# Kernel tuning notes

Measured on AMD Instinct MI355X. Metric: run time of the kernel, lower is better.

Reference implementation:

```python
import jax, jax.numpy as jnp
import numpy as np

D_MODEL = 1024
N_HEADS = 16
D_K = D_MODEL // N_HEADS
T_MIN = 0.01
T_MAX = 2.0
B = 4
S = 1024


def setup_inputs() -> dict:
    key = jax.random.key(0)
    ks = jax.random.split(key, 16)
    sc = 1.0 / np.sqrt(D_MODEL).astype(np.float32)
    inp = {
        'query': jax.random.normal(ks[0], (B, S, D_MODEL), jnp.float32),
        'key': jax.random.normal(ks[1], (B, S, D_MODEL), jnp.float32),
        'value': jax.random.normal(ks[2], (B, S, D_MODEL), jnp.float32),
        # Linear weights stored as (in, out); torch does x @ W.T + b with W (out,in)
        'Wq': jax.random.normal(ks[3], (D_MODEL, D_MODEL), jnp.float32) * sc,
        'bq': jax.random.normal(ks[4], (D_MODEL,), jnp.float32) * 0.01,
        'Wk': jax.random.normal(ks[5], (D_MODEL, D_MODEL), jnp.float32) * sc,
        'bk': jax.random.normal(ks[6], (D_MODEL,), jnp.float32) * 0.01,
        'Wv': jax.random.normal(ks[7], (D_MODEL, D_MODEL), jnp.float32) * sc,
        'bv': jax.random.normal(ks[8], (D_MODEL,), jnp.float32) * 0.01,
        'Wo': jax.random.normal(ks[9], (D_MODEL, D_MODEL), jnp.float32) * sc,
        'bo': jax.random.normal(ks[10], (D_MODEL,), jnp.float32) * 0.01,
        # time-predictor MLP: Linear(3,16) -> tanh -> Linear(16,1)
        'Wt1': jax.random.normal(ks[11], (3, 16), jnp.float32) * 0.5,
        'bt1': jax.random.normal(ks[12], (16,), jnp.float32) * 0.1,
        'Wt2': jax.random.normal(ks[13], (16, 1), jnp.float32) * 0.25,
        'bt2': jax.random.normal(ks[14], (1,), jnp.float32) * 0.1,
    }
    return inp


def _forward(query, key, value, Wq, bq, Wk, bk, Wv, bv, Wo, bo, Wt1, bt1, Wt2, bt2):
    Bq, Sq, D = query.shape
    Sk = key.shape[1]

    def proj(x, W, b, Slen):
        return (x @ W + b).reshape(Bq, Slen, N_HEADS, D_K).transpose(0, 2, 1, 3)

    Q = proj(query, Wq, bq, Sq)   # (B,H,Sq,dk)
    K = proj(key, Wk, bk, Sk)     # (B,H,Sk,dk)
    V = proj(value, Wv, bv, Sk)   # (B,H,Sk,dk)

    # --- DiffusionTimePredictor (fp32) ---
    Qf = Q.astype(jnp.float32)
    Kf = K.astype(jnp.float32)
    inv_sqrt_dk = np.float32(1.0 / np.sqrt(D_K))
    s = jnp.einsum('bhqd,bhkd->bhqk', Qf, Kf) * inv_sqrt_dk
    s = jnp.clip(s, -50.0, 50.0)
    mean_sim = s.mean(axis=(-2, -1))                       # (B,H)
    max_sim = s.max(axis=-1).mean(axis=-1)                 # (B,H)
    probs = jax.nn.softmax(s / 2.0, axis=-1)
    entropy_proxy = probs.var(axis=-1, ddof=1).mean(axis=-1)  # torch var unbiased=True
    mean_sim = jnp.clip(jnp.nan_to_num(mean_sim), -10.0, 10.0)
    max_sim = jnp.clip(jnp.nan_to_num(max_sim), -10.0, 10.0)
    entropy_proxy = jnp.clip(jnp.nan_to_num(entropy_proxy, nan=0.1), 0.0, 1.0)
    feats = jnp.stack([mean_sim, max_sim, entropy_proxy], axis=-1)  # (B,H,3)
    raw_t = jnp.tanh(feats @ Wt1 + bt1) @ Wt2 + bt2                  # (B,H,1)
    t = T_MIN + jax.nn.sigmoid(raw_t) * (T_MAX - T_MIN)
    t = jnp.clip(t, T_MIN, T_MAX)[..., None].astype(query.dtype)     # (B,H,1,1)
    t = jnp.minimum(t, 0.85)                                          # clamp(max=0.85)

    # --- heat kernel attention ---
    scores = jnp.einsum('bhqd,bhkd->bhqk', Q, K) / (2.0 * t)
    attn = jnp.nan_to_num(jax.nn.softmax(scores, axis=-1))
    out = jnp.einsum('bhqk,bhkd->bhqd', attn, V)
    out = out.transpose(0, 2, 1, 3).reshape(Bq, Sq, D)
    return out @ Wo + bo


def reference(query, key, value, Wq, bq, Wk, bk, Wv, bv, Wo, bo, Wt1, bt1, Wt2, bt2):
    return _forward(query, key, value, Wq, bq, Wk, bk, Wv, bv, Wo, bo, Wt1, bt1, Wt2, bt2)
```

## Files before the change

### kernel.cpp

```cpp
#include <hip/hip_runtime.h>
#include <hip/hip_bf16.h>
#include <math.h>

#define SS   1024
#define DM   1024
#define NH   16
#define DKH  64
#define NB   4
#define NBH  64

typedef unsigned short ush;
typedef unsigned int uint32;
typedef __attribute__((ext_vector_type(8))) short bf8_t;
typedef __attribute__((ext_vector_type(4))) float f32x4;
#define MFMA16(a,b,c) __builtin_amdgcn_mfma_f32_16x16x32_bf16((a),(b),(c),0,0,0)

__device__ __forceinline__ ush f2bf(float x){ return __bfloat16_as_ushort(__float2bfloat16(x)); }
__device__ __forceinline__ float bf2f(ush h){ return __bfloat162float(__ushort_as_bfloat16(h)); }
__device__ __forceinline__ uint32 pk2(float a, float b){
  return (uint32)f2bf(a) | ((uint32)f2bf(b) << 16);
}
__device__ __forceinline__ uint32 pkhl(float v){
  ush h = f2bf(v);
  return (uint32)h | ((uint32)f2bf(v - bf2f(h)) << 16);
}
__device__ __forceinline__ uint32 prmh(uint32 uhi, uint32 ulo){
  return __builtin_amdgcn_perm(uhi, ulo, 0x05040100u);
}
__device__ __forceinline__ uint32 prml(uint32 uhi, uint32 ulo){
  return __builtin_amdgcn_perm(uhi, ulo, 0x07060302u);
}
__device__ __forceinline__ int swz8(int row, int chunk){
  return row*64 + (((chunk) ^ (row & 7)) << 3);
}
union U4B8 { uint4 u; bf8_t b; };

__global__ __launch_bounds__(256) void xconv(
    const float* __restrict__ q, const float* __restrict__ k, const float* __restrict__ v,
    ush* __restrict__ xq, ush* __restrict__ xk, ush* __restrict__ xv)
{
  const float* src = (blockIdx.y==0)?q:(blockIdx.y==1)?k:v;
  ush* dst = (blockIdx.y==0)?xq:(blockIdx.y==1)?xk:xv;
  const size_t i = ((size_t)blockIdx.x*256 + threadIdx.x)*8;
  float4 a = *(const float4*)&src[i];
  float4 b = *(const float4*)&src[i+4];
  uint4 o;
  o.x = pk2(a.x, a.y); o.y = pk2(a.z, a.w);
  o.z = pk2(b.x, b.y); o.w = pk2(b.z, b.w);
  *(uint4*)&dst[i] = o;
}

__global__ void wconv4(const float* __restrict__ W0, const float* __restrict__ W1,
                       const float* __restrict__ W2, const float* __restrict__ W3,
                       ush* __restrict__ H0, ush* __restrict__ H1,
                       ush* __restrict__ H2, ush* __restrict__ H3)
{
  __shared__ float T[32][33];
  const int tx = threadIdx.x, ty = threadIdx.y;
  const int z = blockIdx.z;
  const float* W = (z==0)?W0:(z==1)?W1:(z==2)?W2:W3;
  ush* H = (z==0)?H0:(z==1)?H1:(z==2)?H2:H3;
  const int k0 = blockIdx.y*32, n0 = blockIdx.x*32;
  #pragma unroll
  for (int i = 0; i < 4; ++i){
    int r = ty + 8*i;
    T[r][tx] = W[(size_t)(k0 + r)*DM + n0 + tx];
  }
  __syncthreads();
  #pragma unroll
  for (int i = 0; i < 4; ++i){
    int r = ty + 8*i;
    H[(size_t)(n0 + r)*DM + k0 + tx] = f2bf(T[tx][r]);
  }
}

__global__ __launch_bounds__(256) void proj_qkv(
    const ush* __restrict__ xq, const ush* __restrict__ xk, const ush* __restrict__ xv,
    const ush* __restrict__ Wqh, const ush* __restrict__ Wkh, const ush* __restrict__ Wvh,
    const float* __restrict__ bq, const float* __restrict__ bk,
    const float* __restrict__ bv,
    uint32* __restrict__ Qi, ush* __restrict__ Kb, ush* __restrict__ Vt)
{
  __shared__ ush SMEM[16896];

  const int fid = blockIdx.x;
  const int glob = (fid & 7)*96 + (fid >> 3);
  const int z = glob >> 8, rem = glob & 255;
  const int m0 = (rem >> 3) * 128, n0 = (rem & 7) * 128;

  const ush* A  = (z==0) ? xq  : (z==1) ? xk  : xv;
  const ush* Bh = (z==0) ? Wqh : (z==1) ? Wkh : Wvh;

  const int tid = threadIdx.x;
  const int lane = tid & 63, w = tid >> 6;
  const int c = lane & 15, g = lane >> 4;
  const int wr = w >> 1, wc = w & 1;

  f32x4 acc[4][4];
  #pragma unroll
  for (int i = 0; i < 4; ++i)
    #pragma unroll
    for (int j = 0; j < 4; ++j) acc[i][j] = (f32x4){0.f,0.f,0.f,0.f};

  const int prow0 = w*16 + (lane >> 3), prow1 = prow0 + 8;
  const int jj = lane & 7;
  const int sg0 = jj ^ (prow0 & 7), sg1 = jj ^ (prow1 & 7);
  const size_t aoff0 = (size_t)(2*prow0 + (sg0 >> 2))*DM + (sg0 & 3)*8;
  const size_t aoff1 = (size_t)(2*prow1 + (sg1 >> 2))*DM + (sg1 & 3)*8;
  const ush* Aab = A  + (size_t)m0*DM;
  const ush* Bhb = Bh + (size_t)n0*DM;
  const int lb0 = w*1024, lb1 = w*1024 + 512;

#define GLL(GP, LIDX) __builtin_amdgcn_global_load_lds( \
    (const __attribute__((address_space(1))) unsigned int*)(GP), \
    (__attribute__((address_space(3))) unsigned int*)(&SMEM[LIDX]), 16, 0, 0)

#define ISSUE_PROJ(BUFO, KT) do{ \
    GLL(Aab + aoff0 + (KT), (BUFO) + lb0); \
    GLL(Aab + aoff1 + (KT), (BUFO) + lb1); \
    GLL(Bhb + aoff0 + (KT), (BUFO) + 4096 + lb0); \
    GLL(Bhb + aoff1 + (KT), (BUFO) + 4096 + lb1); \
  }while(0)

  const int csw = (((4*(c & 1) + g) ^ ((c >> 1) & 7)) << 3);

  ISSUE_PROJ(0, 0);
  int cur = 0;
  for (int kt = 0; kt < DM; kt += 32){
    __syncthreads();
    if (kt + 32 < DM) ISSUE_PROJ((cur ^ 1)*8192, kt + 32);

    const ush* As  = SMEM + cur*8192;
    const ush* Bhs = As + 4096;

    bf8_t a_h[4];
    #pragma unroll
    for (int fm = 0; fm < 4; ++fm)
      a_h[fm] = *(const bf8_t*)&As[(32*wr + 8*fm + (c>>1))*64 + csw];
    __builtin_amdgcn_s_setprio(1);
    #pragma unroll
    for (int fn = 0; fn < 4; ++fn){
      bf8_t b_h = *(const bf8_t*)&Bhs[(32*wc + 8*fn + (c>>1))*64 + csw];
      #pragma unroll
      for (int fm = 0; fm < 4; ++fm)
        acc[fm][fn] = MFMA16(a_h[fm], b_h, acc[fm][fn]);
    }
    __builtin_amdgcn_s_setprio(0);
    cur ^= 1;
  }
#undef ISSUE_PROJ
#undef GLL

  if (z == 0){
    #pragma unroll
    for (int fm = 0; fm < 4; ++fm){
      #pragma unroll
      for (int fn = 0; fn < 4; ++fn){
        const int col = n0 + 64*wc + 16*fn + c;
        const float bb = bq[col];
        const int row0 = m0 + 64*wr + 16*fm + 4*g;
        const int hd = col >> 6, d = col & 63;
        #pragma unroll
        for (int r = 0; r < 4; ++r){
          const int row = row0 + r;
          const int b = row >> 10, s = row & 1023;
          Qi[((size_t)(b*NH + hd)*SS + s)*DKH + d] = pkhl(acc[fm][fn][r] + bb);
        }
      }
    }
  } else if (z == 1){
    #pragma unroll
    for (int fm = 0; fm < 4; ++fm){
      #pragma unroll
      for (int fn = 0; fn < 4; ++fn){
        const int col = n0 + 64*wc + 16*fn + c;
        const float bb = bk[col];
        const int row0 = m0 + 64*wr + 16*fm + 4*g;
        const int hd = col >> 6, d = col & 63;
        #pragma unroll
        for (int r = 0; r < 4; ++r){
          const int row = row0 + r;
          const int b = row >> 10, s = row & 1023;
          Kb[((size_t)(b*NH + hd)*SS + s)*DKH + d] = f2bf(acc[fm][fn][r] + bb);
        }
      }
    }
  } else {
    __syncthreads();
    ush* Vep = SMEM + w*4224;
    #pragma unroll
    for (int fm = 0; fm < 4; ++fm){
      #pragma unroll
      for (int fn = 0; fn < 4; ++fn){
        const float bb = bv[n0 + 64*wc + 16*fn + c];
        #pragma unroll
        for (int r = 0; r < 4; ++r)
          Vep[(16*fn + c)*66 + 16*fm + 4*g + r] = f2bf(acc[fm][fn][r] + bb);
      }
    }
    const int b = m0 >> 10;
    const int s0 = (m0 & 1023) + 64*wr;
    const int hd = (n0 >> 6) + wc;
    const size_t vbase = ((size_t)(b*NH + hd))*DKH*SS;
    #pragma unroll
    for (int it = 0; it < 8; ++it){
      const int dr = 8*it + (lane >> 3);
      const int sc = (lane & 7)*8;
      uint4 vv = *(const uint4*)&Vep[dr*66 + sc];
      *(uint4*)&Vt[vbase + (size_t)dr*SS + s0 + sc] = vv;
    }
  }
}

__global__ __launch_bounds__(256) void gemm_out(
    const ush* __restrict__ Abf, const ush* __restrict__ Bth,
    const float* __restrict__ bias, float* __restrict__ outf)
{
  __shared__ ush As[4096], Bs[2048];

  const int fid = blockIdx.x;
  const int glob = (fid & 7)*64 + (fid >> 3);
  const int m0 = (glob >> 4)*128, n0 = (glob & 15)*64;

  const int tid = threadIdx.x;
  const int lane = tid & 63, w = tid >> 6;
  const int c = lane & 15, g = lane >> 4;
  const int wr = w >> 1, wc = w & 1;

  f32x4 acc[4][2];
  #pragma unroll
  for (int i = 0; i < 4; ++i){ acc[i][0] = (f32x4){0,0,0,0}; acc[i][1] = (f32x4){0,0,0,0}; }

  const int prow = tid >> 3, ci = tid & 7;
  const int lr   = 2*prow + (ci >> 2);
  const int koff = (ci & 3) << 3;
  const int ws0  = prow*64 + ((ci ^ (prow & 7)) << 3);
  const int ws1  = ws0 + 32*64;
  const int csw  = (((4*(c & 1) + g) ^ ((c >> 1) & 7)) << 3);

  uint4 ar0, ar1, brr;
  #define ISSUE_OUT(KT) do{ \
    ar0 = *(const uint4*)(Abf + (size_t)(m0 + lr)*DM + (KT) + koff); \
    ar1 = *(const uint4*)(Abf + (size_t)(m0 + lr + 64)*DM + (KT) + koff); \
    brr = *(const uint4*)(Bth + (size_t)(n0 + lr)*DM + (KT) + koff); \
  }while(0)

  ISSUE_OUT(0);
  for (int kt = 0; kt < DM; kt += 32){
    *(uint4*)&As[ws0] = ar0;
    *(uint4*)&As[ws1] = ar1;
    if (lr < 64) *(uint4*)&Bs[ws0] = brr;
    __syncthreads();
    if (kt + 32 < DM) ISSUE_OUT(kt + 32);

    bf8_t a_h[4];
    #pragma unroll
    for (int fm = 0; fm < 4; ++fm)
      a_h[fm] = *(const bf8_t*)&As[(32*wr + 8*fm + (c>>1))*64 + csw];
    #pragma unroll
    for (int fn = 0; fn < 2; ++fn){
      bf8_t b_h = *(const bf8_t*)&Bs[(16*wc + 8*fn + (c>>1))*64 + csw];
      #pragma unroll
      for (int fm = 0; fm < 4; ++fm)
        acc[fm][fn] = MFMA16(a_h[fm], b_h, acc[fm][fn]);
    }
    __syncthreads();
  }
  #undef ISSUE_OUT

  #pragma unroll
  for (int fm = 0; fm < 4; ++fm){
    #pragma unroll
    for (int fn = 0; fn < 2; ++fn){
      const int col = n0 + 32*wc + 16*fn + c;
      const float bb = bias[col];
      const int row0 = m0 + 64*wr + 16*fm + 4*g;
      #pragma unroll
      for (int r = 0; r < 4; ++r)
        outf[(size_t)(row0 + r)*DM + col] = acc[fm][fn][r] + bb;
    }
  }
}

__global__ __launch_bounds__(512) void attn_stats_mfma(
    const uint32* __restrict__ Qi, const ush* __restrict__ Kb,
    float* __restrict__ stats, unsigned int* __restrict__ cnt,
    const float* __restrict__ Wt1, const float* __restrict__ bt1,
    const float* __restrict__ Wt2, const float* __restrict__ bt2,
    float* __restrict__ tws)
{
  __shared__ ush Khs[128*64];
  __shared__ float red[8][3];
  const int tid = threadIdx.x, lane = tid & 63, w = tid >> 6;
  const int c = lane & 15, g = lane >> 4;
  const int fid = blockIdx.x;
  const int glob = (fid & 7)*64 + (fid >> 3);
  const int bh = glob >> 3, q0 = (glob & 7)*128;

  bf8_t qh[2];
  {
    const size_t qoff = ((size_t)bh*SS + q0 + 16*w + c)*DKH + 8*g;
    uint4 u0 = *(const uint4*)(Qi + qoff);
    uint4 u1 = *(const uint4*)(Qi + qoff + 4);
    uint4 u2 = *(const uint4*)(Qi + qoff + 32);
    uint4 u3 = *(const uint4*)(Qi + qoff + 36);
    U4B8 t;
    t.u = (uint4){prmh(u0.y,u0.x), prmh(u0.w,u0.z), prmh(u1.y,u1.x), prmh(u1.w,u1.z)}; qh[0] = t.b;
    t.u = (uint4){prmh(u2.y,u2.x), prmh(u2.w,u2.z), prmh(u3.y,u3.x), prmh(u3.w,u3.z)}; qh[1] = t.b;
  }

  float ssum = 0.f, rmax = -1e30f, lsum = 0.f, l2sum = 0.f;
  const int rrK = tid >> 2, chK = (tid & 3)*2;

  uint4 k0, k1;
  #define ISSUE_ST(KC) do{ \
    const ush* kp = Kb + ((size_t)bh*SS + (KC)*128 + rrK)*DKH + chK*8; \
    k0 = *(const uint4*)(kp); \
    k1 = *(const uint4*)(kp + 8); \
  }while(0)

  ISSUE_ST(0);
  for (int kc = 0; kc < 8; ++kc){
    *(uint4*)&Khs[rrK*64 + (((chK + 0) ^ (rrK & 7)) << 3)] = k0;
    *(uint4*)&Khs[rrK*64 + (((chK + 1) ^ (rrK & 7)) << 3)] = k1;
    __syncthreads();
    if (kc < 7) ISSUE_ST(kc + 1);

    f32x4 sa[8];
    #pragma unroll
    for (int fn = 0; fn < 8; ++fn) sa[fn] = (f32x4){0.f,0.f,0.f,0.f};
    __builtin_amdgcn_s_setprio(1);
    #pragma unroll
    for (int fn = 0; fn < 8; ++fn){
      #pragma unroll
      for (int ds = 0; ds < 2; ++ds){
        bf8_t ah = *(const bf8_t*)&Khs[(16*fn + c)*64 + (((g + 4*ds) ^ (c & 7)) << 3)];
        sa[fn] = MFMA16(ah, qh[ds], sa[fn]);
      }
    }
    __builtin_amdgcn_s_setprio(0);
    #pragma unroll
    for (int fn = 0; fn < 8; ++fn){
      #pragma unroll
      for (int r = 0; r < 4; ++r){
        float s = sa[fn][r] * 0.125f;
        ssum += s;
        rmax = fmaxf(rmax, s);
        float e = exp2f(s * 0.7213475204f);
        lsum += e;
        l2sum = fmaf(e, e, l2sum);
      }
    }
    __syncthreads();
  }
  #undef ISSUE_ST

  rmax  = fmaxf(rmax, __shfl_xor(rmax, 16, 64));
  rmax  = fmaxf(rmax, __shfl_xor(rmax, 32, 64));
  lsum  += __shfl_xor(lsum, 16, 64);   lsum  += __shfl_xor(lsum, 32, 64);
  l2sum += __shfl_xor(l2sum, 16, 64);  l2sum += __shfl_xor(l2sum, 32, 64);
  float varc = (l2sum/(lsum*lsum) - (1.0f/1024.f)) * (1.0f/1023.f);
  float a0 = ssum, a1 = rmax * 0.25f, a2 = varc * 0.25f;
  #pragma unroll
  for (int off = 1; off < 64; off <<= 1){
    a0 += __shfl_xor(a0, off, 64);
    a1 += __shfl_xor(a1, off, 64);
    a2 += __shfl_xor(a2, off, 64);
  }
  if (lane == 0){ red[w][0] = a0; red[w][1] = a1; red[w][2] = a2; }
  __syncthreads();
  if (tid == 0){
    float r0 = 0.f, r1 = 0.f, r2 = 0.f;
    #pragma unroll
    for (int i = 0; i < 8; ++i){ r0 += red[i][0]; r1 += red[i][1]; r2 += red[i][2]; }
    atomicAdd(&stats[bh*4+0], r0);
    atomicAdd(&stats[bh*4+1], r1);
    atomicAdd(&stats[bh*4+2], r2);
    __threadfence();
    if (atomicAdd(&cnt[bh], 1u) == 7u){
      float v0 = atomicAdd(&stats[bh*4+0], 0.f);
      float v1 = atomicAdd(&stats[bh*4+1], 0.f);
      float v2 = atomicAdd(&stats[bh*4+2], 0.f);
      float mean = fminf(fmaxf(v0 * (1.f/(1024.f*1024.f)), -10.f), 10.f);
      float mx   = fminf(fmaxf(v1 * (1.f/1024.f), -10.f), 10.f);
      float ent  = fminf(fmaxf(v2 * (1.f/1024.f),   0.f),  1.f);
      float raw = bt2[0];
      #pragma unroll
      for (int j = 0; j < 16; ++j){
        float h = tanhf(mean*Wt1[j] + mx*Wt1[16+j] + ent*Wt1[32+j] + bt1[j]);
        raw += h * Wt2[j];
      }
      float sig = 1.f / (1.f + expf(-raw));
      float t = 0.01f + sig * 1.99f;
      t = fminf(fminf(fmaxf(t, 0.01f), 2.0f), 0.85f);
      tws[bh] = t;
    }
  }
}

__global__ __launch_bounds__(512) void attn_flash_mfma(
    const uint32* __restrict__ Qi, const ush* __restrict__ Kb,
    const ush* __restrict__ Vt, const float* __restrict__ tws,
    ush* __restrict__ aout)
{
  __shared__ ush Khs[128*64], Vts[64*128], Ps[128*128];
  const int tid = threadIdx.x, lane = tid & 63, w = tid >> 6;
  const int c = lane & 15, g = lane >> 4;
  const int fid = blockIdx.x;
  const int glob = (fid & 7)*64 + (fid >> 3);
  const int bh = glob >> 3, q0 = (glob & 7)*128;
  const float tsc2 = (0.5f / tws[bh]) * 1.44269504f;

  bf8_t qh[2], ql[2];
  {
    const size_t qoff = ((size_t)bh*SS + q0 + 16*w + c)*DKH + 8*g;
    uint4 u0 = *(const uint4*)(Qi + qoff);
    uint4 u1 = *(const uint4*)(Qi + qoff + 4);
    uint4 u2 = *(const uint4*)(Qi + qoff + 32);
    uint4 u3 = *(const uint4*)(Qi + qoff + 36);
    U4B8 t;
    t.u = (uint4){prmh(u0.y,u0.x), prmh(u0.w,u0.z), prmh(u1.y,u1.x), prmh(u1.w,u1.z)}; qh[0] = t.b;
    t.u = (uint4){prml(u0.y,u0.x), prml(u0.w,u0.z), prml(u1.y,u1.x), prml(u1.w,u1.z)}; ql[0] = t.b;
    t.u = (uint4){prmh(u2.y,u2.x), prmh(u2.w,u2.z), prmh(u3.y,u3.x), prmh(u3.w,u3.z)}; qh[1] = t.b;
    t.u = (uint4){prml(u2.y,u2.x), prml(u2.w,u2.z), prml(u3.y,u3.x), prml(u3.w,u3.z)}; ql[1] = t.b;
  }

  f32x4 o[4];
  #pragma unroll
  for (int i = 0; i < 4; ++i) o[i] = (f32x4){0.f,0.f,0.f,0.f};
  float m = -INFINITY, lpart = 0.f;

  const int rrK = tid >> 2, chK = (tid & 3)*2;
  const int rrV = tid >> 3, chV = (tid & 7)*2;

  uint4 k0, k1, v0, v1;
  #define ISSUE_FL(KC) do{ \
    const ush* kp = Kb + ((size_t)bh*SS + (KC)*128 + rrK)*DKH + chK*8; \
    k0 = *(const uint4*)(kp); \
    k1 = *(const uint4*)(kp + 8); \
    const ush* vp = Vt + ((size_t)bh*DKH + rrV)*SS + (KC)*128 + chV*8; \
    v0 = *(const uint4*)(vp); \
    v1 = *(const uint4*)(vp + 8); \
  }while(0)

  ISSUE_FL(0);
  for (int kc = 0; kc < 8; ++kc){
    *(uint4*)&Khs[rrK*64  + (((chK + 0) ^ (rrK & 7)) << 3)] = k0;
    *(uint4*)&Khs[rrK*64  + (((chK + 1) ^ (rrK & 7)) << 3)] = k1;
    *(uint4*)&Vts[rrV*128 + (((chV + 0) ^ (rrV & 7)) << 3)] = v0;
    *(uint4*)&Vts[rrV*128 + (((chV + 1) ^ (rrV & 7)) << 3)] = v1;
    __syncthreads();
    if (kc < 7) ISSUE_FL(kc + 1);

    f32x4 sa[8];
    #pragma unroll
    for (int fn = 0; fn < 8; ++fn) sa[fn] = (f32x4){0.f,0.f,0.f,0.f};
    __builtin_amdgcn_s_setprio(1);
    #pragma unroll
    for (int fn = 0; fn < 8; ++fn){
      #pragma unroll
      for (int ds = 0; ds < 2; ++ds){
        bf8_t ah = *(const bf8_t*)&Khs[(16*fn + c)*64 + (((g + 4*ds) ^ (c & 7)) << 3)];
        sa[fn] = MFMA16(ah, qh[ds], sa[fn]);
        sa[fn] = MFMA16(ah, ql[ds], sa[fn]);
      }
    }
    __builtin_amdgcn_s_setprio(0);

    float pmaxr = -1e30f;
    #pragma unroll
    for (int fn = 0; fn < 8; ++fn)
      #pragma unroll
      for (int r = 0; r < 4; ++r) pmaxr = fmaxf(pmaxr, sa[fn][r]);

    if (!__all(pmaxr * tsc2 <= m + 30.f)){
      pmaxr = fmaxf(pmaxr, __shfl_xor(pmaxr, 16, 64));
      pmaxr = fmaxf(pmaxr, __shfl_xor(pmaxr, 32, 64));
      float pmax = pmaxr * tsc2;
      float mn = fmaxf(m, pmax);
      float sc = exp2f(m - mn);
      m = mn;
      lpart *= sc;
      #pragma unroll
      for (int r = 0; r < 4; ++r){
        float so = __shfl(sc, 4*g + r, 16);
        #pragma unroll
        for (int fn = 0; fn < 4; ++fn) o[fn][r] *= so;
      }
    }

    const float mneg = -m;
    #pragma unroll
    for (int fn = 0; fn < 8; ++fn){
      float e0 = exp2f(fmaf(sa[fn][0], tsc2, mneg));
      float e1 = exp2f(fmaf(sa[fn][1], tsc2, mneg));
      float e2 = exp2f(fmaf(sa[fn][2], tsc2, mneg));
      float e3 = exp2f(fmaf(sa[fn][3], tsc2, mneg));
      lpart += (e0 + e1) + (e2 + e3);
      uint2 pk;
      pk.x = pk2(e0, e1);
      pk.y = pk2(e2, e3);
      const int q4 = 4*fn + g;
      const int addr = (16*w + c)*128 + ((((q4 >> 1) ^ (c & 7)) << 3)) + (q4 & 1)*4;
      *(uint2*)&Ps[addr] = pk;
    }

    __builtin_amdgcn_s_setprio(1);
    #pragma unroll
    for (int kvs = 0; kvs < 4; ++kvs){
      bf8_t pa = *(const bf8_t*)&Ps[(16*w + c)*128 + (((g + 4*kvs) ^ (c & 7)) << 3)];
      #pragma unroll
      for (int fn = 0; fn < 4; ++fn){
        bf8_t vb = *(const bf8_t*)&Vts[(16*fn + c)*128 + (((g + 4*kvs) ^ (c & 7)) << 3)];
        o[fn] = MFMA16(pa, vb, o[fn]);
      }
    }
    __builtin_amdgcn_s_setprio(0);
    __syncthreads();
  }
  #undef ISSUE_FL

  lpart += __shfl_xor(lpart, 16, 64);
  lpart += __shfl_xor(lpart, 32, 64);
  const int b = bh >> 4, hd = bh & 15;
  #pragma unroll
  for (int r = 0; r < 4; ++r){
    float linv = 1.f / __shfl(lpart, 4*g + r, 16);
    const int q = q0 + 16*w + 4*g + r;
    #pragma unroll
    for (int fn = 0; fn < 4; ++fn)
      aout[((size_t)(b*SS + q))*DM + hd*DKH + 16*fn + c] = f2bf(o[fn][r] * linv);
  }
}

extern "C" void kernel_launch(void* const* d_in, const int* in_sizes, int n_in,
                              void* d_out, int out_size, void* d_ws, size_t ws_size,
                              hipStream_t stream)
{
  const float* query = (const float*)d_in[0];
  const float* key   = (const float*)d_in[1];
  const float* value = (const float*)d_in[2];
  const float* Wq = (const float*)d_in[3];
  const float* bq = (const float*)d_in[4];
  const float* Wk = (const float*)d_in[5];
  const float* bk = (const float*)d_in[6];
  const float* Wv = (const float*)d_in[7];
  const float* bv = (const float*)d_in[8];
  const float* Wo = (const float*)d_in[9];
  const float* bo = (const float*)d_in[10];
  const float* Wt1 = (const float*)d_in[11];
  const float* bt1 = (const float*)d_in[12];
  const float* Wt2 = (const float*)d_in[13];
  const float* bt2 = (const float*)d_in[14];

  const size_t E = (size_t)NB*SS*DM;
  const size_t WE = (size_t)DM*DM;

  uint32* Qi  = (uint32*)d_ws;
  ush* Kbb = (ush*)(Qi + E);
  ush* Vtb = Kbb + E;
  ush* Aob = Vtb + E;
  ush* xqb = Aob;
  ush* xkb = Aob + E;
  ush* xvb = xkb + E;
  ush* Wqh = xvb + E;
  ush* Wkh = Wqh + WE;
  ush* Wvh = Wkh + WE;
  ush* Woh = Wvh + WE;
  float* stats = (float*)(Woh + WE);
  unsigned int* cnt = (unsigned int*)(stats + 4*NBH);
  float* tws   = (float*)(cnt + NBH);

  hipMemsetAsync(stats, 0, (4*NBH + NBH)*sizeof(float), stream);

  xconv<<<dim3(2048, 3), 256, 0, stream>>>(query, key, value, xqb, xkb, xvb);

  dim3 wb(32, 8), wg(32, 32, 4);
  wconv4<<<wg, wb, 0, stream>>>(Wq, Wk, Wv, Wo, Wqh, Wkh, Wvh, Woh);

  proj_qkv<<<768, 256, 0, stream>>>(xqb, xkb, xvb,
      Wqh, Wkh, Wvh, bq, bk, bv, Qi, Kbb, Vtb);

  attn_stats_mfma<<<512, 512, 0, stream>>>(Qi, Kbb, stats, cnt,
      Wt1, bt1, Wt2, bt2, tws);
  attn_flash_mfma<<<512, 512, 0, stream>>>(Qi, Kbb, Vtb, tws, Aob);

  gemm_out<<<512, 256, 0, stream>>>(Aob, Woh, bo, (float*)d_out);
}
```

Measured before the change: 164.9 us.

## Split time-MLP into separate kernel and shrink stats K tile to 64 rows

Removes the last-block-done counter, threadfence and atomic readback from the stats kernel and computes the time-predictor MLP in a small separate kernel launch. It also halves the shared K tile in the stats kernel (64 rows per step, 16 steps) using a swizzle helper, which lowers LDS use and per-step register pressure. The cost is one extra kernel launch and twice as many barrier iterations in the stats loop.

```diff
diff --git a/kernel.cpp b/kernel.cpp
--- a/kernel.cpp
+++ b/kernel.cpp
@@ -284,12 +284,9 @@
 
 __global__ __launch_bounds__(512) void attn_stats_mfma(
     const uint32* __restrict__ Qi, const ush* __restrict__ Kb,
-    float* __restrict__ stats, unsigned int* __restrict__ cnt,
-    const float* __restrict__ Wt1, const float* __restrict__ bt1,
-    const float* __restrict__ Wt2, const float* __restrict__ bt2,
-    float* __restrict__ tws)
-{
-  __shared__ ush Khs[128*64];
+    float* __restrict__ stats)
+{
+  __shared__ ush Khs[64*64];
   __shared__ float red[8][3];
   const int tid = threadIdx.x, lane = tid & 63, w = tid >> 6;
   const int c = lane & 15, g = lane >> 4;
@@ -310,37 +307,34 @@
   }
 
   float ssum = 0.f, rmax = -1e30f, lsum = 0.f, l2sum = 0.f;
-  const int rrK = tid >> 2, chK = (tid & 3)*2;
-
-  uint4 k0, k1;
+  const int rr0 = tid >> 3, ci = tid & 7;
+
+  uint4 k0;
   #define ISSUE_ST(KC) do{ \
-    const ush* kp = Kb + ((size_t)bh*SS + (KC)*128 + rrK)*DKH + chK*8; \
-    k0 = *(const uint4*)(kp); \
-    k1 = *(const uint4*)(kp + 8); \
+    k0 = *(const uint4*)(Kb + ((size_t)bh*SS + (KC)*64 + rr0)*DKH + ci*8); \
   }while(0)
 
   ISSUE_ST(0);
-  for (int kc = 0; kc < 8; ++kc){
-    *(uint4*)&Khs[rrK*64 + (((chK + 0) ^ (rrK & 7)) << 3)] = k0;
-    *(uint4*)&Khs[rrK*64 + (((chK + 1) ^ (rrK & 7)) << 3)] = k1;
-    __syncthreads();
-    if (kc < 7) ISSUE_ST(kc + 1);
-
-    f32x4 sa[8];
-    #pragma unroll
-    for (int fn = 0; fn < 8; ++fn) sa[fn] = (f32x4){0.f,0.f,0.f,0.f};
+  for (int kc = 0; kc < 16; ++kc){
+    *(uint4*)&Khs[swz8(rr0, ci)] = k0;
+    __syncthreads();
+    if (kc < 15) ISSUE_ST(kc + 1);
+
+    f32x4 sa[4];
+    #pragma unroll
+    for (int fn = 0; fn < 4; ++fn) sa[fn] = (f32x4){0.f,0.f,0.f,0.f};
     __builtin_amdgcn_s_setprio(1);
     #pragma unroll
-    for (int fn = 0; fn < 8; ++fn){
+    for (int fn = 0; fn < 4; ++fn){
       #pragma unroll
       for (int ds = 0; ds < 2; ++ds){
-        bf8_t ah = *(const bf8_t*)&Khs[(16*fn + c)*64 + (((g + 4*ds) ^ (c & 7)) << 3)];
+        bf8_t ah = *(const bf8_t*)&Khs[swz8(16*fn + c, g + 4*ds)];
         sa[fn] = MFMA16(ah, qh[ds], sa[fn]);
       }
     }
     __builtin_amdgcn_s_setprio(0);
     #pragma unroll
-    for (int fn = 0; fn < 8; ++fn){
+    for (int fn = 0; fn < 4; ++fn){
       #pragma unroll
       for (int r = 0; r < 4; ++r){
         float s = sa[fn][r] * 0.125f;
@@ -376,26 +370,29 @@
     atomicAdd(&stats[bh*4+0], r0);
     atomicAdd(&stats[bh*4+1], r1);
     atomicAdd(&stats[bh*4+2], r2);
-    __threadfence();
-    if (atomicAdd(&cnt[bh], 1u) == 7u){
-      float v0 = atomicAdd(&stats[bh*4+0], 0.f);
-      float v1 = atomicAdd(&stats[bh*4+1], 0.f);
-      float v2 = atomicAdd(&stats[bh*4+2], 0.f);
-      float mean = fminf(fmaxf(v0 * (1.f/(1024.f*1024.f)), -10.f), 10.f);
-      float mx   = fminf(fmaxf(v1 * (1.f/1024.f), -10.f), 10.f);
-      float ent  = fminf(fmaxf(v2 * (1.f/1024.f),   0.f),  1.f);
-      float raw = bt2[0];
-      #pragma unroll
-      for (int j = 0; j < 16; ++j){
-        float h = tanhf(mean*Wt1[j] + mx*Wt1[16+j] + ent*Wt1[32+j] + bt1[j]);
-        raw += h * Wt2[j];
-      }
-      float sig = 1.f / (1.f + expf(-raw));
-      float t = 0.01f + sig * 1.99f;
-      t = fminf(fminf(fmaxf(t, 0.01f), 2.0f), 0.85f);
-      tws[bh] = t;
-    }
-  }
+  }
+}
+
+__global__ void time_mlp(const float* __restrict__ stats,
+    const float* __restrict__ Wt1, const float* __restrict__ bt1,
+    const float* __restrict__ Wt2, const float* __restrict__ bt2,
+    float* __restrict__ tws)
+{
+  int bh = threadIdx.x;
+  if (bh >= NBH) return;
+  float mean = fminf(fmaxf(stats[bh*4+0] * (1.f/(1024.f*1024.f)), -10.f), 10.f);
+  float mx   = fminf(fmaxf(stats[bh*4+1] * (1.f/1024.f), -10.f), 10.f);
+  float ent  = fminf(fmaxf(stats[bh*4+2] * (1.f/1024.f),   0.f),  1.f);
+  float raw = bt2[0];
+  #pragma unroll
+  for (int j = 0; j < 16; ++j){
+    float h = tanhf(mean*Wt1[j] + mx*Wt1[16+j] + ent*Wt1[32+j] + bt1[j]);
+    raw += h * Wt2[j];
+  }
+  float sig = 1.f / (1.f + expf(-raw));
+  float t = 0.01f + sig * 1.99f;
+  t = fminf(fminf(fmaxf(t, 0.01f), 2.0f), 0.85f);
+  tws[bh] = t;
 }
 
 __global__ __launch_bounds__(512) void attn_flash_mfma(
@@ -568,10 +565,9 @@
   ush* Wvh = Wkh + WE;
   ush* Woh = Wvh + WE;
   float* stats = (float*)(Woh + WE);
-  unsigned int* cnt = (unsigned int*)(stats + 4*NBH);
-  float* tws   = (float*)(cnt + NBH);
-
-  hipMemsetAsync(stats, 0, (4*NBH + NBH)*sizeof(float), stream);
+  float* tws   = stats + 4*NBH;
+
+  hipMemsetAsync(stats, 0, 4*NBH*sizeof(float), stream);
 
   xconv<<<dim3(2048, 3), 256, 0, stream>>>(query, key, value, xqb, xkb, xvb);
 
@@ -581,8 +577,8 @@
   proj_qkv<<<768, 256, 0, stream>>>(xqb, xkb, xvb,
       Wqh, Wkh, Wvh, bq, bk, bv, Qi, Kbb, Vtb);
 
-  attn_stats_mfma<<<512, 512, 0, stream>>>(Qi, Kbb, stats, cnt,
-      Wt1, bt1, Wt2, bt2, tws);
+  attn_stats_mfma<<<512, 512, 0, stream>>>(Qi, Kbb, stats);
+  time_mlp<<<1, 64, 0, stream>>>(stats, Wt1, bt1, Wt2, bt2, tws);
   attn_flash_mfma<<<512, 512, 0, stream>>>(Qi, Kbb, Vtb, tws, Aob);
 
   gemm_out<<<512, 256, 0, stream>>>(Aob, Woh, bo, (float*)d_out);
```

Measured after the change: 152.2 us. -7.7%, faster.
